# Performance work log

Measured on AMD Instinct MI355X. Metric: run time of the kernel, lower is better.

Reference implementation:

```python
import jax, jax.numpy as jnp
import numpy as np

ALPHA = 1000.0  # softmin temperature from the original module


def setup_inputs() -> dict:
    key = jax.random.key(0)
    ks = jax.random.split(key, 10)
    B, D, H, E, K = 8192, 784, 256, 32, 512
    s = 0.05  # small init scale to keep activations/distances numerically sane
    return {
        "x": jax.random.normal(ks[0], (B, D), jnp.float32),
        "cluster_reps": jax.random.normal(ks[1], (K, E), jnp.float32),
        "W1": jax.random.normal(ks[2], (D, H), jnp.float32) * s,
        "b1": jnp.zeros((H,), jnp.float32),
        "W2": jax.random.normal(ks[3], (H, E), jnp.float32) * s,
        "b2": jnp.zeros((E,), jnp.float32),
        "W3": jax.random.normal(ks[4], (E, H), jnp.float32) * s,
        "b3": jnp.zeros((H,), jnp.float32),
        "W4": jax.random.normal(ks[5], (H, D), jnp.float32) * s,
        "b4": jnp.zeros((D,), jnp.float32),
    }


def reference(x, cluster_reps, W1, b1, W2, b2, W3, b3, W4, b4):
    # --- autoencoder: 2-layer MLP encoder / decoder ---
    h = jax.nn.relu(x @ W1 + b1)            # [B, H]
    embeddings = h @ W2 + b2                # [B, E]
    h2 = jax.nn.relu(embeddings @ W3 + b3)  # [B, H]
    reconstruction = h2 @ W4 + b4           # [B, D]

    # --- squared distances to cluster reps: [B, K] ---
    diff = embeddings[:, None, :] - cluster_reps[None, :, :]  # [B, K, E]
    distances = jnp.sum(diff * diff, axis=2)                  # [B, K]

    # --- stable softmin-weighted distances ---
    min_dist = jnp.min(distances, axis=1, keepdims=True)       # [B, 1]
    exponentials = jnp.exp(-ALPHA * (distances - min_dist))    # [B, K]
    sum_exponentials = jnp.sum(exponentials, axis=1, keepdims=True)
    weighted_dists = distances * (exponentials / sum_exponentials)

    return (weighted_dists, distances, reconstruction, embeddings)
```

## Files before the change

### kernel.cpp

```cpp
#include <hip/hip_runtime.h>
#include <cstddef>

#define NB 8192
#define ND 784
#define NH 256
#define NE 32
#define NK 512
#define ALPHA_F 1000.0f

typedef _Float16 h8 __attribute__((ext_vector_type(8)));
typedef float f32x4 __attribute__((ext_vector_type(4)));

__global__ __launch_bounds__(256)
void splitw2_kernel(const float* __restrict__ W1, _Float16* __restrict__ w1thi,
                    _Float16* __restrict__ w1tlo,
                    const float* __restrict__ W4, _Float16* __restrict__ w4thi,
                    _Float16* __restrict__ w4tlo) {
    const int b = blockIdx.x;
    const float* W; _Float16 *hi, *lo; int K, N, n;
    if (b < NH) { W = W1; hi = w1thi; lo = w1tlo; K = ND; N = NH; n = b; }
    else        { W = W4; hi = w4thi; lo = w4tlo; K = NH; N = ND; n = b - NH; }
    for (int k = threadIdx.x; k < K; k += 256) {
        float w = W[(size_t)k * N + n];
        _Float16 hh = (_Float16)w;
        float r = w - (float)hh;
        hi[(size_t)n * K + k] = hh;
        lo[(size_t)n * K + k] = (_Float16)(r * 2048.0f);
    }
}

template<int TERMS, bool RELU, bool SPLITA, int MT>
__global__ __launch_bounds__(256)
void mfma_gemm3(const float* __restrict__ Af32,
                const _Float16* __restrict__ Ahi_g,
                const _Float16* __restrict__ Alo_g,
                const _Float16* __restrict__ WThi,
                const _Float16* __restrict__ WTlo,
                const float* __restrict__ bias, float* __restrict__ C,
                int N, int K, int KS) {
    constexpr int BM  = MT * 32;
    constexpr int ACH = BM / 64;

    __shared__ _Float16 sAhi[2][BM * 40];
    __shared__ _Float16 sAlo[2][BM * 40];
    __shared__ _Float16 sBhi[2][64 * 40];
    __shared__ _Float16 sBlo[2][64 * 40];

    const int tid = threadIdx.x;
    const int bm  = blockIdx.x * BM;
    const int bn  = blockIdx.y * 64;

    const int arow = (ACH == 1) ? (tid >> 2) : (tid >> 1);
    const int ak   = (ACH == 1) ? ((tid & 3) * 8) : ((tid & 1) * 16);
    const int brow = tid >> 2;
    const int bk   = (tid & 3) * 8;

    const float*    pA32 = SPLITA ? Af32 + (size_t)(bm + arow) * K : nullptr;
    const _Float16* pAhi = SPLITA ? nullptr : Ahi_g + (size_t)(bm + arow) * K;
    const _Float16* pAlo = SPLITA ? nullptr : Alo_g + (size_t)(bm + arow) * K;
    int brow_g = bn + brow; if (brow_g > N - 1) brow_g = N - 1;
    const _Float16* pBhi = WThi + (size_t)brow_g * K;
    const _Float16* pBlo = WTlo + (size_t)brow_g * K;

    float araw[ACH * 8];
    h8 rahi[ACH], ralo[ACH];
    h8 rbhi, rblo;

    auto prefetch = [&](int s) {
        #pragma unroll
        for (int c = 0; c < ACH; ++c) {
            const int k = s * 32 + ak + c * 8;
            if (SPLITA) {
                if (k + 8 <= K) {
                    f32x4 v0 = *(const f32x4*)(pA32 + k);
                    f32x4 v1 = *(const f32x4*)(pA32 + k + 4);
                    #pragma unroll
                    for (int j = 0; j < 4; ++j) {
                        araw[c * 8 + j]     = v0[j];
                        araw[c * 8 + 4 + j] = v1[j];
                    }
                } else {
                    #pragma unroll
                    for (int j = 0; j < 8; ++j) araw[c * 8 + j] = 0.f;
                }
            } else {
                rahi[c] = (k + 8 <= K) ? *(const h8*)(pAhi + k) : (h8){};
                ralo[c] = (k + 8 <= K) ? *(const h8*)(pAlo + k) : (h8){};
            }
        }
        const int kb = s * 32 + bk;
        rbhi = (kb + 8 <= K) ? *(const h8*)(pBhi + kb) : (h8){};
        rblo = (kb + 8 <= K) ? *(const h8*)(pBlo + kb) : (h8){};
    };

    auto commit = [&](int buf) {
        #pragma unroll
        for (int c = 0; c < ACH; ++c) {
            h8 hi, lo;
            if (SPLITA) {
                #pragma unroll
                for (int j = 0; j < 8; ++j) {
                    float v = araw[c * 8 + j];
                    _Float16 hh = (_Float16)v;
                    hi[j] = hh;
                    lo[j] = (_Float16)((v - (float)hh) * 2048.0f);
                }
            } else { hi = rahi[c]; lo = ralo[c]; }
            *(h8*)&sAhi[buf][arow * 40 + ak + c * 8] = hi;
            *(h8*)&sAlo[buf][arow * 40 + ak + c * 8] = lo;
        }
        *(h8*)&sBhi[buf][brow * 40 + bk] = rbhi;
        *(h8*)&sBlo[buf][brow * 40 + bk] = rblo;
    };

    prefetch(0);
    commit(0);
    prefetch(1);
    __syncthreads();

    const int lane = tid & 63;
    const int wv   = tid >> 6;
    const int wm   = (wv >> 1) * (MT * 16);
    const int wn   = (wv & 1) * 32;
    const int li   = lane & 15;
    const int kq   = (lane >> 4) * 8;

    f32x4 acc0[MT][2] = {};
    f32x4 acc1[MT][2] = {};
    f32x4 acc2[MT][2] = {};

    for (int s = 0; s < KS; ++s) {
        const int buf = s & 1;
        h8 fahi[MT], falo[MT], fbhi[2], fblo[2];
        #pragma unroll
        for (int mt = 0; mt < MT; ++mt) {
            const int ao = (wm + mt * 16 + li) * 40 + kq;
            fahi[mt] = *(const h8*)&sAhi[buf][ao];
            falo[mt] = *(const h8*)&sAlo[buf][ao];
        }
        #pragma unroll
        for (int nt = 0; nt < 2; ++nt) {
            const int bo = (wn + nt * 16 + li) * 40 + kq;
            fbhi[nt] = *(const h8*)&sBhi[buf][bo];
            fblo[nt] = *(const h8*)&sBlo[buf][bo];
        }
        #pragma unroll
        for (int mt = 0; mt < MT; ++mt)
            #pragma unroll
            for (int nt = 0; nt < 2; ++nt) {
                acc0[mt][nt] = __builtin_amdgcn_mfma_f32_16x16x32_f16(
                    fahi[mt], fbhi[nt], acc0[mt][nt], 0, 0, 0);
                acc1[mt][nt] = __builtin_amdgcn_mfma_f32_16x16x32_f16(
                    fahi[mt], fblo[nt], acc1[mt][nt], 0, 0, 0);
                acc1[mt][nt] = __builtin_amdgcn_mfma_f32_16x16x32_f16(
                    falo[mt], fbhi[nt], acc1[mt][nt], 0, 0, 0);
                if (TERMS == 4)
                    acc2[mt][nt] = __builtin_amdgcn_mfma_f32_16x16x32_f16(
                        falo[mt], fblo[nt], acc2[mt][nt], 0, 0, 0);
            }
        if (s + 1 < KS) {
            commit((s + 1) & 1);
            if (s + 2 < KS) prefetch(s + 2);
        }
        __syncthreads();
    }

    const float c1 = 1.0f / 2048.0f;
    const float c2 = c1 * c1;
    const int quad = lane >> 4;
    #pragma unroll
    for (int nt = 0; nt < 2; ++nt) {
        const int n = bn + wn + nt * 16 + li;
        if (n < N) {
            const float bv = bias[n];
            #pragma unroll
            for (int mt = 0; mt < MT; ++mt) {
                #pragma unroll
                for (int r = 0; r < 4; ++r) {
                    const int m = bm + wm + mt * 16 + quad * 4 + r;
                    float v = acc0[mt][nt][r] + c1 * acc1[mt][nt][r];
                    if (TERMS == 4) v += c2 * acc2[mt][nt][r];
                    v += bv;
                    if (RELU) v = fmaxf(v, 0.f);
                    C[(size_t)m * N + n] = v;
                }
            }
        }
    }
}

__global__ __launch_bounds__(256)
void mid_kernel(const float* __restrict__ h, const float* __restrict__ W2,
                const float* __restrict__ b2, const float* __restrict__ W3,
                const float* __restrict__ b3, float* __restrict__ emb,
                _Float16* __restrict__ h2hi, _Float16* __restrict__ h2lo) {
    __shared__ float es[16][32];
    const int tid = threadIdx.x;
    const int r0  = blockIdx.x * 16;

    #pragma unroll
    for (int half = 0; half < 2; ++half) {
        const int o   = tid + half * 256;
        const int row = o >> 5;
        const int col = o & 31;
        const float* hrow = h + (size_t)(r0 + row) * NH;
        float acc0 = 0.f, acc1 = 0.f;
        #pragma unroll 4
        for (int k = 0; k < NH; k += 4) {
            float4 hv = *(const float4*)(hrow + k);
            acc0 = fmaf(hv.x, W2[(k + 0) * NE + col], acc0);
            acc1 = fmaf(hv.y, W2[(k + 1) * NE + col], acc1);
            acc0 = fmaf(hv.z, W2[(k + 2) * NE + col], acc0);
            acc1 = fmaf(hv.w, W2[(k + 3) * NE + col], acc1);
        }
        float v = acc0 + acc1 + b2[col];
        es[row][col] = v;
        emb[(size_t)r0 * NE + o] = v;
    }
    __syncthreads();

    const int col = tid;
    float acc[16];
    #pragma unroll
    for (int r = 0; r < 16; ++r) acc[r] = 0.f;
    #pragma unroll
    for (int k = 0; k < NE; ++k) {
        float w = W3[k * NH + col];
        #pragma unroll
        for (int r = 0; r < 16; ++r) acc[r] = fmaf(es[r][k], w, acc[r]);
    }
    const float bb = b3[col];
    #pragma unroll
    for (int r = 0; r < 16; ++r) {
        float v = acc[r] + bb;
        v = v > 0.f ? v : 0.f;
        _Float16 hh = (_Float16)v;
        float rr = v - (float)hh;
        h2hi[(size_t)(r0 + r) * NH + col] = hh;
        h2lo[(size_t)(r0 + r) * NH + col] = (_Float16)(rr * 2048.0f);
    }
}

__global__ __launch_bounds__(512, 4)
void dist_kernel(const float* __restrict__ emb, const float* __restrict__ reps,
                 float* __restrict__ dist, float* __restrict__ wout) {
    __shared__ float es[8][32];
    __shared__ float tr[8][520];
    __shared__ float rmin[8];
    __shared__ float rinv[8];

    const int tid = threadIdx.x;
    const int r0  = blockIdx.x * 8;

    if (tid < 256) es[tid >> 5][tid & 31] = emb[(size_t)r0 * NE + tid];

    const float* rp = reps + (size_t)tid * NE;
    f32x4 rv[8];
    #pragma unroll
    for (int e4 = 0; e4 < 8; ++e4) rv[e4] = ((const f32x4*)rp)[e4];
    __syncthreads();

    float d[8];
    #pragma unroll
    for (int r = 0; r < 8; ++r) {
        float a = 0.f;
        #pragma unroll
        for (int e4 = 0; e4 < 8; ++e4) {
            f32x4 ev = *(const f32x4*)&es[r][e4 * 4];
            #pragma unroll
            for (int j = 0; j < 4; ++j) {
                float t = ev[j] - rv[e4][j];
                a = fmaf(t, t, a);
            }
        }
        d[r] = a;
    }

    const int lane = tid & 63;
    const int wv   = tid >> 6;

    #pragma unroll
    for (int r = 0; r < 8; ++r) tr[r][tid] = d[r];
    __syncthreads();
    {
        f32x4 a = *(const f32x4*)&tr[wv][lane * 8];
        f32x4 b = *(const f32x4*)&tr[wv][lane * 8 + 4];
        float m = fminf(fminf(fminf(a[0], a[1]), fminf(a[2], a[3])),
                        fminf(fminf(b[0], b[1]), fminf(b[2], b[3])));
        #pragma unroll
        for (int off = 32; off > 0; off >>= 1)
            m = fminf(m, __shfl_xor(m, off, 64));
        if (lane == 0) rmin[wv] = m;
    }
    __syncthreads();

    float e[8];
    #pragma unroll
    for (int r = 0; r < 8; ++r) {
        e[r] = expf(-ALPHA_F * (d[r] - rmin[r]));
        tr[r][tid] = e[r];
    }
    __syncthreads();
    {
        f32x4 a = *(const f32x4*)&tr[wv][lane * 8];
        f32x4 b = *(const f32x4*)&tr[wv][lane * 8 + 4];
        float s = ((a[0] + a[1]) + (a[2] + a[3])) +
                  ((b[0] + b[1]) + (b[2] + b[3]));
        #pragma unroll
        for (int off = 32; off > 0; off >>= 1)
            s += __shfl_xor(s, off, 64);
        if (lane == 0) rinv[wv] = 1.0f / s;
    }
    __syncthreads();

    #pragma unroll
    for (int r = 0; r < 8; ++r) {
        const size_t row = (size_t)(r0 + r);
        dist[row * NK + tid] = d[r];
        wout[row * NK + tid] = d[r] * (e[r] * rinv[r]);
    }
}

extern "C" void kernel_launch(void* const* d_in, const int* in_sizes, int n_in,
                              void* d_out, int out_size, void* d_ws, size_t ws_size,
                              hipStream_t stream) {
    const float* x    = (const float*)d_in[0];
    const float* reps = (const float*)d_in[1];
    const float* W1   = (const float*)d_in[2];
    const float* b1   = (const float*)d_in[3];
    const float* W2   = (const float*)d_in[4];
    const float* b2   = (const float*)d_in[5];
    const float* W3   = (const float*)d_in[6];
    const float* b3   = (const float*)d_in[7];
    const float* W4   = (const float*)d_in[8];
    const float* b4   = (const float*)d_in[9];

    float* out   = (float*)d_out;
    float* wout  = out;
    float* dist  = out + (size_t)NB * NK;
    float* recon = out + (size_t)2 * NB * NK;
    float* emb   = out + (size_t)2 * NB * NK + (size_t)NB * ND;

    float*    h     = dist;
    _Float16* h2hi  = (_Float16*)(dist + (size_t)NB * NH);
    _Float16* h2lo  = h2hi + (size_t)NB * NH;
    _Float16* w1thi = (_Float16*)wout;
    _Float16* w1tlo = w1thi + (size_t)NH * ND;
    _Float16* w4thi = w1tlo + (size_t)NH * ND;
    _Float16* w4tlo = w4thi + (size_t)ND * NH;

    splitw2_kernel<<<NH + ND, 256, 0, stream>>>(W1, w1thi, w1tlo,
                                                W4, w4thi, w4tlo);

    mfma_gemm3<4, true, true, 2><<<dim3(128, 4), 256, 0, stream>>>(
        x, nullptr, nullptr, w1thi, w1tlo, b1, h, NH, ND, 25);

    mid_kernel<<<NB / 16, 256, 0, stream>>>(h, W2, b2, W3, b3, emb, h2hi, h2lo);

    mfma_gemm3<3, false, false, 4><<<dim3(64, 13), 256, 0, stream>>>(
        nullptr, h2hi, h2lo, w4thi, w4tlo, b4, recon, ND, NH, 8);

    dist_kernel<<<NB / 8, 512, 0, stream>>>(emb, reps, dist, wout);
}
```

Before: 181.2 us.

## Fuse recon GEMM and distance/softmin into one heterogeneous tail kernel

Moves the split weights and h2 buffers into workspace so the distance kernel no longer has to wait for the recon GEMM to finish using the output buffers. Both can then run in one launch whose blocks interleave GEMM tiles and 256-thread distance tiles, overlapping the compute-bound GEMM with the memory-bound distance/softmin work. This saves one kernel launch and the tail of the GEMM. The cost is that every block reserves the larger GEMM shared-memory footprint and uses a uniform 256-thread size, which may lower occupancy for the distance blocks. It also depends on a large enough workspace, with the old path kept as a fallback.

```diff
diff --git a/kernel.cpp b/kernel.cpp
--- a/kernel.cpp
+++ b/kernel.cpp
@@ -30,25 +30,23 @@
 }
 
 template<int TERMS, bool RELU, bool SPLITA, int MT>
-__global__ __launch_bounds__(256)
-void mfma_gemm3(const float* __restrict__ Af32,
-                const _Float16* __restrict__ Ahi_g,
-                const _Float16* __restrict__ Alo_g,
-                const _Float16* __restrict__ WThi,
-                const _Float16* __restrict__ WTlo,
-                const float* __restrict__ bias, float* __restrict__ C,
-                int N, int K, int KS) {
+__device__ __forceinline__ void gemm_body(
+    const float* __restrict__ Af32,
+    const _Float16* __restrict__ Ahi_g,
+    const _Float16* __restrict__ Alo_g,
+    const _Float16* __restrict__ WThi,
+    const _Float16* __restrict__ WTlo,
+    const float* __restrict__ bias, float* __restrict__ C,
+    int N, int K, int KS, int bx, int by, int tid,
+    _Float16* __restrict__ sAhi, _Float16* __restrict__ sAlo,
+    _Float16* __restrict__ sBhi, _Float16* __restrict__ sBlo) {
     constexpr int BM  = MT * 32;
     constexpr int ACH = BM / 64;
-
-    __shared__ _Float16 sAhi[2][BM * 40];
-    __shared__ _Float16 sAlo[2][BM * 40];
-    __shared__ _Float16 sBhi[2][64 * 40];
-    __shared__ _Float16 sBlo[2][64 * 40];
-
-    const int tid = threadIdx.x;
-    const int bm  = blockIdx.x * BM;
-    const int bn  = blockIdx.y * 64;
+    constexpr int AS  = BM * 40;
+    constexpr int BS  = 64 * 40;
+
+    const int bm = bx * BM;
+    const int bn = by * 64;
 
     const int arow = (ACH == 1) ? (tid >> 2) : (tid >> 1);
     const int ak   = (ACH == 1) ? ((tid & 3) * 8) : ((tid & 1) * 16);
@@ -106,11 +104,11 @@
                     lo[j] = (_Float16)((v - (float)hh) * 2048.0f);
                 }
             } else { hi = rahi[c]; lo = ralo[c]; }
-            *(h8*)&sAhi[buf][arow * 40 + ak + c * 8] = hi;
-            *(h8*)&sAlo[buf][arow * 40 + ak + c * 8] = lo;
-        }
-        *(h8*)&sBhi[buf][brow * 40 + bk] = rbhi;
-        *(h8*)&sBlo[buf][brow * 40 + bk] = rblo;
+            *(h8*)&sAhi[buf * AS + arow * 40 + ak + c * 8] = hi;
+            *(h8*)&sAlo[buf * AS + arow * 40 + ak + c * 8] = lo;
+        }
+        *(h8*)&sBhi[buf * BS + brow * 40 + bk] = rbhi;
+        *(h8*)&sBlo[buf * BS + brow * 40 + bk] = rblo;
     };
 
     prefetch(0);
@@ -134,15 +132,15 @@
         h8 fahi[MT], falo[MT], fbhi[2], fblo[2];
         #pragma unroll
         for (int mt = 0; mt < MT; ++mt) {
-            const int ao = (wm + mt * 16 + li) * 40 + kq;
-            fahi[mt] = *(const h8*)&sAhi[buf][ao];
-            falo[mt] = *(const h8*)&sAlo[buf][ao];
+            const int ao = buf * AS + (wm + mt * 16 + li) * 40 + kq;
+            fahi[mt] = *(const h8*)&sAhi[ao];
+            falo[mt] = *(const h8*)&sAlo[ao];
         }
         #pragma unroll
         for (int nt = 0; nt < 2; ++nt) {
-            const int bo = (wn + nt * 16 + li) * 40 + kq;
-            fbhi[nt] = *(const h8*)&sBhi[buf][bo];
-            fblo[nt] = *(const h8*)&sBlo[buf][bo];
+            const int bo = buf * BS + (wn + nt * 16 + li) * 40 + kq;
+            fbhi[nt] = *(const h8*)&sBhi[bo];
+            fblo[nt] = *(const h8*)&sBlo[bo];
         }
         #pragma unroll
         for (int mt = 0; mt < MT; ++mt)
@@ -189,6 +187,26 @@
     }
 }
 
+template<int TERMS, bool RELU, bool SPLITA, int MT>
+__global__ __launch_bounds__(256)
+void mfma_gemm3(const float* __restrict__ Af32,
+                const _Float16* __restrict__ Ahi_g,
+                const _Float16* __restrict__ Alo_g,
+                const _Float16* __restrict__ WThi,
+                const _Float16* __restrict__ WTlo,
+                const float* __restrict__ bias, float* __restrict__ C,
+                int N, int K, int KS) {
+    constexpr int BM = MT * 32;
+    __shared__ __align__(16) _Float16 smem[2 * BM * 40 * 2 + 2 * 64 * 40 * 2];
+    _Float16* sAhi = smem;
+    _Float16* sAlo = sAhi + 2 * BM * 40;
+    _Float16* sBhi = sAlo + 2 * BM * 40;
+    _Float16* sBlo = sBhi + 2 * 64 * 40;
+    gemm_body<TERMS, RELU, SPLITA, MT>(Af32, Ahi_g, Alo_g, WThi, WTlo, bias, C,
+                                       N, K, KS, blockIdx.x, blockIdx.y,
+                                       threadIdx.x, sAhi, sAlo, sBhi, sBlo);
+}
+
 __global__ __launch_bounds__(256)
 void mid_kernel(const float* __restrict__ h, const float* __restrict__ W2,
                 const float* __restrict__ b2, const float* __restrict__ W3,
@@ -241,6 +259,98 @@
     }
 }
 
+__device__ __forceinline__ void dist_body256(
+    const float* __restrict__ emb, const float* __restrict__ reps,
+    float* __restrict__ dist, float* __restrict__ wout,
+    int blk, int tid, float* __restrict__ es, float* __restrict__ tr,
+    float* __restrict__ rmin, float* __restrict__ rinv) {
+    const int r0 = blk * 8;
+    es[tid] = emb[(size_t)r0 * NE + tid];
+
+    const float* rp0 = reps + (size_t)tid * NE;
+    const float* rp1 = reps + (size_t)(tid + 256) * NE;
+    f32x4 rv0[8], rv1[8];
+    #pragma unroll
+    for (int e4 = 0; e4 < 8; ++e4) {
+        rv0[e4] = ((const f32x4*)rp0)[e4];
+        rv1[e4] = ((const f32x4*)rp1)[e4];
+    }
+    __syncthreads();
+
+    float d0[8], d1[8];
+    #pragma unroll
+    for (int r = 0; r < 8; ++r) {
+        float a0 = 0.f, a1 = 0.f;
+        #pragma unroll
+        for (int e4 = 0; e4 < 8; ++e4) {
+            f32x4 ev = *(const f32x4*)&es[r * 32 + e4 * 4];
+            #pragma unroll
+            for (int j = 0; j < 4; ++j) {
+                float t0 = ev[j] - rv0[e4][j];
+                a0 = fmaf(t0, t0, a0);
+                float t1 = ev[j] - rv1[e4][j];
+                a1 = fmaf(t1, t1, a1);
+            }
+        }
+        d0[r] = a0; d1[r] = a1;
+    }
+
+    const int lane = tid & 63;
+    const int wv   = tid >> 6;
+
+    #pragma unroll
+    for (int r = 0; r < 8; ++r) {
+        tr[r * 520 + tid]       = d0[r];
+        tr[r * 520 + 256 + tid] = d1[r];
+    }
+    __syncthreads();
+    #pragma unroll
+    for (int p = 0; p < 2; ++p) {
+        const int rr = wv + p * 4;
+        f32x4 a = *(const f32x4*)&tr[rr * 520 + lane * 8];
+        f32x4 b = *(const f32x4*)&tr[rr * 520 + lane * 8 + 4];
+        float m = fminf(fminf(fminf(a[0], a[1]), fminf(a[2], a[3])),
+                        fminf(fminf(b[0], b[1]), fminf(b[2], b[3])));
+        #pragma unroll
+        for (int off = 32; off > 0; off >>= 1)
+            m = fminf(m, __shfl_xor(m, off, 64));
+        if (lane == 0) rmin[rr] = m;
+    }
+    __syncthreads();
+
+    float e0[8], e1[8];
+    #pragma unroll
+    for (int r = 0; r < 8; ++r) {
+        e0[r] = expf(-ALPHA_F * (d0[r] - rmin[r]));
+        e1[r] = expf(-ALPHA_F * (d1[r] - rmin[r]));
+        tr[r * 520 + tid]       = e0[r];
+        tr[r * 520 + 256 + tid] = e1[r];
+    }
+    __syncthreads();
+    #pragma unroll
+    for (int p = 0; p < 2; ++p) {
+        const int rr = wv + p * 4;
+        f32x4 a = *(const f32x4*)&tr[rr * 520 + lane * 8];
+        f32x4 b = *(const f32x4*)&tr[rr * 520 + lane * 8 + 4];
+        float s = ((a[0] + a[1]) + (a[2] + a[3])) +
+                  ((b[0] + b[1]) + (b[2] + b[3]));
+        #pragma unroll
+        for (int off = 32; off > 0; off >>= 1)
+            s += __shfl_xor(s, off, 64);
+        if (lane == 0) rinv[rr] = 1.0f / s;
+    }
+    __syncthreads();
+
+    #pragma unroll
+    for (int r = 0; r < 8; ++r) {
+        const size_t row = (size_t)(r0 + r);
+        dist[row * NK + tid]       = d0[r];
+        dist[row * NK + 256 + tid] = d1[r];
+        wout[row * NK + tid]       = d0[r] * (e0[r] * rinv[r]);
+        wout[row * NK + 256 + tid] = d1[r] * (e1[r] * rinv[r]);
+    }
+}
+
 __global__ __launch_bounds__(512, 4)
 void dist_kernel(const float* __restrict__ emb, const float* __restrict__ reps,
                  float* __restrict__ dist, float* __restrict__ wout) {
@@ -318,6 +428,42 @@
         const size_t row = (size_t)(r0 + r);
         dist[row * NK + tid] = d[r];
         wout[row * NK + tid] = d[r] * (e[r] * rinv[r]);
+    }
+}
+
+#define NGB (64 * 13)
+#define NDB (NB / 8)
+
+__global__ __launch_bounds__(256)
+void tail_fused(const _Float16* __restrict__ h2hi,
+                const _Float16* __restrict__ h2lo,
+                const _Float16* __restrict__ w4thi,
+                const _Float16* __restrict__ w4tlo,
+                const float* __restrict__ b4, float* __restrict__ recon,
+                const float* __restrict__ emb, const float* __restrict__ reps,
+                float* __restrict__ dist, float* __restrict__ wout) {
+    __shared__ __align__(16) _Float16 smem[2 * 128 * 40 * 2 + 2 * 64 * 40 * 2];
+    const int bid = blockIdx.x;
+    const int tid = threadIdx.x;
+
+    bool isDist; int idx;
+    if (bid < 2 * NGB) { isDist = (bid & 1); idx = bid >> 1; }
+    else               { isDist = true; idx = NGB + (bid - 2 * NGB); }
+
+    if (!isDist) {
+        _Float16* sAhi = smem;
+        _Float16* sAlo = sAhi + 2 * 128 * 40;
+        _Float16* sBhi = sAlo + 2 * 128 * 40;
+        _Float16* sBlo = sBhi + 2 * 64 * 40;
+        gemm_body<3, false, false, 4>(nullptr, h2hi, h2lo, w4thi, w4tlo, b4,
+                                      recon, ND, NH, 8, idx & 63, idx >> 6,
+                                      tid, sAhi, sAlo, sBhi, sBlo);
+    } else {
+        float* es   = (float*)smem;
+        float* tr   = es + 8 * 32;
+        float* rmin = tr + 8 * 520;
+        float* rinv = rmin + 8;
+        dist_body256(emb, reps, dist, wout, idx, tid, es, tr, rmin, rinv);
     }
 }
 
@@ -341,24 +487,43 @@
     float* recon = out + (size_t)2 * NB * NK;
     float* emb   = out + (size_t)2 * NB * NK + (size_t)NB * ND;
 
-    float*    h     = dist;
-    _Float16* h2hi  = (_Float16*)(dist + (size_t)NB * NH);
-    _Float16* h2lo  = h2hi + (size_t)NB * NH;
-    _Float16* w1thi = (_Float16*)wout;
-    _Float16* w1tlo = w1thi + (size_t)NH * ND;
-    _Float16* w4thi = w1tlo + (size_t)NH * ND;
-    _Float16* w4tlo = w4thi + (size_t)ND * NH;
-
-    splitw2_kernel<<<NH + ND, 256, 0, stream>>>(W1, w1thi, w1tlo,
-                                                W4, w4thi, w4tlo);
-
-    mfma_gemm3<4, true, true, 2><<<dim3(128, 4), 256, 0, stream>>>(
-        x, nullptr, nullptr, w1thi, w1tlo, b1, h, NH, ND, 25);
-
-    mid_kernel<<<NB / 16, 256, 0, stream>>>(h, W2, b2, W3, b3, emb, h2hi, h2lo);
-
-    mfma_gemm3<3, false, false, 4><<<dim3(64, 13), 256, 0, stream>>>(
-        nullptr, h2hi, h2lo, w4thi, w4tlo, b4, recon, ND, NH, 8);
-
-    dist_kernel<<<NB / 8, 512, 0, stream>>>(emb, reps, dist, wout);
-}
+    float* h = dist;
+
+    const size_t wneed = ((size_t)4 * ND * NH + (size_t)2 * NB * NH)
+                         * sizeof(_Float16);
+
+    if (d_ws != nullptr && ws_size >= wneed) {
+        _Float16* w1thi = (_Float16*)d_ws;
+        _Float16* w1tlo = w1thi + (size_t)NH * ND;
+        _Float16* w4thi = w1tlo + (size_t)NH * ND;
+        _Float16* w4tlo = w4thi + (size_t)ND * NH;
+        _Float16* h2hi  = w4tlo + (size_t)ND * NH;
+        _Float16* h2lo  = h2hi + (size_t)NB * NH;
+
+        splitw2_kernel<<<NH + ND, 256, 0, stream>>>(W1, w1thi, w1tlo,
+                                                    W4, w4thi, w4tlo);
+        mfma_gemm3<4, true, true, 2><<<dim3(128, 4), 256, 0, stream>>>(
+            x, nullptr, nullptr, w1thi, w1tlo, b1, h, NH, ND, 25);
+        mid_kernel<<<NB / 16, 256, 0, stream>>>(h, W2, b2, W3, b3,
+                                                emb, h2hi, h2lo);
+        tail_fused<<<2 * NGB + (NDB - NGB), 256, 0, stream>>>(
+            h2hi, h2lo, w4thi, w4tlo, b4, recon, emb, reps, dist, wout);
+    } else {
+        _Float16* h2hi  = (_Float16*)(dist + (size_t)NB * NH);
+        _Float16* h2lo  = h2hi + (size_t)NB * NH;
+        _Float16* w1thi = (_Float16*)wout;
+        _Float16* w1tlo = w1thi + (size_t)NH * ND;
+        _Float16* w4thi = w1tlo + (size_t)NH * ND;
+        _Float16* w4tlo = w4thi + (size_t)ND * NH;
+
+        splitw2_kernel<<<NH + ND, 256, 0, stream>>>(W1, w1thi, w1tlo,
+                                                    W4, w4thi, w4tlo);
+        mfma_gemm3<4, true, true, 2><<<dim3(128, 4), 256, 0, stream>>>(
+            x, nullptr, nullptr, w1thi, w1tlo, b1, h, NH, ND, 25);
+        mid_kernel<<<NB / 16, 256, 0, stream>>>(h, W2, b2, W3, b3,
+                                                emb, h2hi, h2lo);
+        mfma_gemm3<3, false, false, 4><<<dim3(64, 13), 256, 0, stream>>>(
+            nullptr, h2hi, h2lo, w4thi, w4tlo, b4, recon, ND, NH, 8);
+        dist_kernel<<<NB / 8, 512, 0, stream>>>(emb, reps, dist, wout);
+    }
+}
```

Result: faster. 176.9 us (-2.4%).

## Fuse entire autoencoder and softmin pipeline into one persistent mega kernel

Applied to the files above, without the earlier changes.

Replaces the chain of four kernels with one prep kernel that splits all four weight matrices into fp16 hi/lo pairs in workspace using an LDS-tiled transpose, plus a single fused kernel. Each 512-thread block owns 32 rows and runs the encoder, embedding, decoder GEMMs and the distance/softmin stage entirely in LDS. This removes intermediate global round-trips (h, h2, emb reload) and launch gaps, at the cost of very large LDS use, one block per CU, only 256 blocks, and recomputing W4 tile loads per block. The old path remains as a fallback when no workspace is available.

```diff
diff --git a/kernel.cpp b/kernel.cpp
--- a/kernel.cpp
+++ b/kernel.cpp
@@ -10,6 +10,434 @@
 
 typedef _Float16 h8 __attribute__((ext_vector_type(8)));
 typedef float f32x4 __attribute__((ext_vector_type(4)));
+
+#define TW1 25
+#define TN1 8
+#define NBW1 200
+#define TW4 8
+#define TN4 25
+#define NBW4 200
+#define NBW2 8
+#define NBW3 8
+
+__global__ __launch_bounds__(256)
+void prep4_kernel(const float* __restrict__ W1, _Float16* __restrict__ w1thi,
+                  _Float16* __restrict__ w1tlo,
+                  const float* __restrict__ W4, _Float16* __restrict__ w4thi,
+                  _Float16* __restrict__ w4tlo,
+                  const float* __restrict__ W2, _Float16* __restrict__ w2thi,
+                  _Float16* __restrict__ w2tlo,
+                  const float* __restrict__ W3, _Float16* __restrict__ w3thi,
+                  _Float16* __restrict__ w3tlo) {
+    __shared__ float tile[32][33];
+    const int b   = blockIdx.x;
+    const int tid = threadIdx.x;
+
+    const float* W; _Float16 *hi, *lo; int K, N, kt, nt;
+    if (b < NBW1) {
+        W = W1; hi = w1thi; lo = w1tlo; K = ND; N = NH;
+        kt = b % TW1; nt = b / TW1;
+    } else if (b < NBW1 + NBW4) {
+        const int bb = b - NBW1;
+        W = W4; hi = w4thi; lo = w4tlo; K = NH; N = ND;
+        kt = bb % TW4; nt = bb / TW4;
+    } else if (b < NBW1 + NBW4 + NBW2) {
+        W = W2; hi = w2thi; lo = w2tlo; K = NH; N = NE;
+        kt = b - (NBW1 + NBW4); nt = 0;
+    } else {
+        W = W3; hi = w3thi; lo = w3tlo; K = NE; N = NH;
+        kt = 0; nt = b - (NBW1 + NBW4 + NBW2);
+    }
+    const int k0 = kt * 32, n0 = nt * 32;
+    const int row = tid >> 3, c4 = (tid & 7) * 4;
+    #pragma unroll
+    for (int j = 0; j < 4; ++j) {
+        const int k = k0 + row, n = n0 + c4 + j;
+        tile[row][c4 + j] = (k < K && n < N) ? W[(size_t)k * N + n] : 0.f;
+    }
+    __syncthreads();
+    const int n = n0 + row;
+    if (n < N) {
+        #pragma unroll
+        for (int j = 0; j < 4; ++j) {
+            const int k = k0 + c4 + j;
+            if (k < K) {
+                float w = tile[c4 + j][row];
+                _Float16 hh = (_Float16)w;
+                float r = w - (float)hh;
+                hi[(size_t)n * K + k] = hh;
+                lo[(size_t)n * K + k] = (_Float16)(r * 2048.0f);
+            }
+        }
+    }
+}
+
+__global__ __launch_bounds__(512, 1)
+void mega_kernel(const float* __restrict__ x, const float* __restrict__ reps,
+                 const _Float16* __restrict__ w1thi, const _Float16* __restrict__ w1tlo,
+                 const _Float16* __restrict__ w2thi, const _Float16* __restrict__ w2tlo,
+                 const _Float16* __restrict__ w3thi, const _Float16* __restrict__ w3tlo,
+                 const _Float16* __restrict__ w4thi, const _Float16* __restrict__ w4tlo,
+                 const float* __restrict__ b1, const float* __restrict__ b2,
+                 const float* __restrict__ b3, const float* __restrict__ b4,
+                 float* __restrict__ emb_g, float* __restrict__ recon_g,
+                 float* __restrict__ dist_g, float* __restrict__ wout_g) {
+    __shared__ __align__(16) unsigned char lds[135936];
+    _Float16* R0h  = (_Float16*)lds;
+    _Float16* sA   = (_Float16*)(lds + 81920);
+    _Float16* hP   = (_Float16*)(lds + 92160);
+    float*    es   = (float*)(lds + 125952);
+    _Float16* eP   = (_Float16*)(lds + 130560);
+    float*    rmin = (float*)(lds + 135680);
+    float*    rinv = (float*)(lds + 135808);
+
+    const int tid  = threadIdx.x;
+    const int lane = tid & 63;
+    const int wv   = tid >> 6;
+    const int li   = lane & 15;
+    const int kq   = (lane >> 4) * 8;
+    const int quad = lane >> 4;
+    const int r0   = blockIdx.x * 32;
+
+    const float c1 = 1.0f / 2048.0f;
+    const float c2 = c1 * c1;
+
+    {
+        _Float16* sBhi = R0h;
+        _Float16* sBlo = R0h + 2 * 256 * 40;
+        _Float16* sAhi = sA;
+        _Float16* sAlo = sA + 2 * 32 * 40;
+        const int arow = (tid & 127) >> 2;
+        const int ak   = (tid & 3) * 8;
+        const int brow = tid >> 1;
+        const int bk   = (tid & 1) * 16;
+        const float*    pA  = x + (size_t)(r0 + arow) * ND;
+        const _Float16* pBh = w1thi + (size_t)brow * ND;
+        const _Float16* pBl = w1tlo + (size_t)brow * ND;
+
+        float araw[8];
+        h8 rb0, rb1, rb2, rb3;
+
+        auto pf = [&](int s) {
+            if (tid < 128) {
+                const int k = s * 32 + ak;
+                if (k + 8 <= ND) {
+                    f32x4 v0 = *(const f32x4*)(pA + k);
+                    f32x4 v1 = *(const f32x4*)(pA + k + 4);
+                    #pragma unroll
+                    for (int j = 0; j < 4; ++j) {
+                        araw[j] = v0[j]; araw[4 + j] = v1[j];
+                    }
+                } else {
+                    #pragma unroll
+                    for (int j = 0; j < 8; ++j) araw[j] = 0.f;
+                }
+            }
+            const int kb = s * 32 + bk;
+            rb0 = (kb + 8  <= ND) ? *(const h8*)(pBh + kb)     : (h8){};
+            rb1 = (kb + 16 <= ND) ? *(const h8*)(pBh + kb + 8) : (h8){};
+            rb2 = (kb + 8  <= ND) ? *(const h8*)(pBl + kb)     : (h8){};
+            rb3 = (kb + 16 <= ND) ? *(const h8*)(pBl + kb + 8) : (h8){};
+        };
+        auto cm = [&](int buf) {
+            if (tid < 128) {
+                h8 hi, lo;
+                #pragma unroll
+                for (int j = 0; j < 8; ++j) {
+                    float v = araw[j];
+                    _Float16 hh = (_Float16)v;
+                    hi[j] = hh;
+                    lo[j] = (_Float16)((v - (float)hh) * 2048.0f);
+                }
+                *(h8*)&sAhi[buf * 32 * 40 + arow * 40 + ak] = hi;
+                *(h8*)&sAlo[buf * 32 * 40 + arow * 40 + ak] = lo;
+            }
+            *(h8*)&sBhi[buf * 256 * 40 + brow * 40 + bk]     = rb0;
+            *(h8*)&sBhi[buf * 256 * 40 + brow * 40 + bk + 8] = rb1;
+            *(h8*)&sBlo[buf * 256 * 40 + brow * 40 + bk]     = rb2;
+            *(h8*)&sBlo[buf * 256 * 40 + brow * 40 + bk + 8] = rb3;
+        };
+
+        pf(0); cm(0); pf(1);
+        __syncthreads();
+
+        f32x4 a0[2][2] = {}, a1[2][2] = {}, a2[2][2] = {};
+        for (int s = 0; s < 25; ++s) {
+            const int buf = s & 1;
+            h8 fah[2], fal[2], fbh[2], fbl[2];
+            #pragma unroll
+            for (int mt = 0; mt < 2; ++mt) {
+                const int ao = buf * 32 * 40 + (mt * 16 + li) * 40 + kq;
+                fah[mt] = *(const h8*)&sAhi[ao];
+                fal[mt] = *(const h8*)&sAlo[ao];
+            }
+            #pragma unroll
+            for (int nt = 0; nt < 2; ++nt) {
+                const int bo = buf * 256 * 40 + (wv * 32 + nt * 16 + li) * 40 + kq;
+                fbh[nt] = *(const h8*)&sBhi[bo];
+                fbl[nt] = *(const h8*)&sBlo[bo];
+            }
+            #pragma unroll
+            for (int mt = 0; mt < 2; ++mt)
+                #pragma unroll
+                for (int nt = 0; nt < 2; ++nt) {
+                    a0[mt][nt] = __builtin_amdgcn_mfma_f32_16x16x32_f16(
+                        fah[mt], fbh[nt], a0[mt][nt], 0, 0, 0);
+                    a1[mt][nt] = __builtin_amdgcn_mfma_f32_16x16x32_f16(
+                        fah[mt], fbl[nt], a1[mt][nt], 0, 0, 0);
+                    a1[mt][nt] = __builtin_amdgcn_mfma_f32_16x16x32_f16(
+                        fal[mt], fbh[nt], a1[mt][nt], 0, 0, 0);
+                    a2[mt][nt] = __builtin_amdgcn_mfma_f32_16x16x32_f16(
+                        fal[mt], fbl[nt], a2[mt][nt], 0, 0, 0);
+                }
+            if (s + 1 < 25) { cm((s + 1) & 1); if (s + 2 < 25) pf(s + 2); }
+            __syncthreads();
+        }
+        _Float16* hhi = hP;
+        _Float16* hlo = hP + 32 * 264;
+        #pragma unroll
+        for (int nt = 0; nt < 2; ++nt) {
+            const int n = wv * 32 + nt * 16 + li;
+            const float bv = b1[n];
+            #pragma unroll
+            for (int mt = 0; mt < 2; ++mt)
+                #pragma unroll
+                for (int r = 0; r < 4; ++r) {
+                    const int m = mt * 16 + quad * 4 + r;
+                    float v = a0[mt][nt][r] + c1 * a1[mt][nt][r]
+                            + c2 * a2[mt][nt][r] + bv;
+                    v = fmaxf(v, 0.f);
+                    _Float16 hh = (_Float16)v;
+                    hhi[m * 264 + n] = hh;
+                    hlo[m * 264 + n] = (_Float16)((v - (float)hh) * 2048.0f);
+                }
+        }
+    }
+    __syncthreads();
+
+    {
+        _Float16* w2h = R0h;
+        _Float16* w2l = R0h + 32 * 264;
+        #pragma unroll
+        for (int i = 0; i < 2; ++i) {
+            const int cc  = tid + i * 512;
+            const int row = cc >> 5, off = (cc & 31) * 8;
+            *(h8*)&w2h[row * 264 + off] = *(const h8*)(w2thi + row * 256 + off);
+            *(h8*)&w2l[row * 264 + off] = *(const h8*)(w2tlo + row * 256 + off);
+        }
+    }
+    __syncthreads();
+    if (wv < 4) {
+        const int mt = wv >> 1, nt = wv & 1;
+        _Float16* hhi = hP;
+        _Float16* hlo = hP + 32 * 264;
+        _Float16* w2h = R0h;
+        _Float16* w2l = R0h + 32 * 264;
+        f32x4 e0 = {}, e1 = {}, e2 = {};
+        #pragma unroll
+        for (int ks = 0; ks < 8; ++ks) {
+            h8 ah = *(const h8*)&hhi[(mt * 16 + li) * 264 + ks * 32 + kq];
+            h8 al = *(const h8*)&hlo[(mt * 16 + li) * 264 + ks * 32 + kq];
+            h8 bh = *(const h8*)&w2h[(nt * 16 + li) * 264 + ks * 32 + kq];
+            h8 bl = *(const h8*)&w2l[(nt * 16 + li) * 264 + ks * 32 + kq];
+            e0 = __builtin_amdgcn_mfma_f32_16x16x32_f16(ah, bh, e0, 0, 0, 0);
+            e1 = __builtin_amdgcn_mfma_f32_16x16x32_f16(ah, bl, e1, 0, 0, 0);
+            e1 = __builtin_amdgcn_mfma_f32_16x16x32_f16(al, bh, e1, 0, 0, 0);
+            e2 = __builtin_amdgcn_mfma_f32_16x16x32_f16(al, bl, e2, 0, 0, 0);
+        }
+        const int ccol = nt * 16 + li;
+        const float bv = b2[ccol];
+        _Float16* ehi = eP;
+        _Float16* elo = eP + 32 * 40;
+        #pragma unroll
+        for (int r = 0; r < 4; ++r) {
+            const int m = mt * 16 + quad * 4 + r;
+            float v = e0[r] + c1 * e1[r] + c2 * e2[r] + bv;
+            es[m * 36 + ccol] = v;
+            _Float16 hh = (_Float16)v;
+            ehi[m * 40 + ccol] = hh;
+            elo[m * 40 + ccol] = (_Float16)((v - (float)hh) * 2048.0f);
+            emb_g[(size_t)(r0 + m) * NE + ccol] = v;
+        }
+    }
+    __syncthreads();
+
+    {
+        _Float16* w3h = R0h;
+        _Float16* w3l = R0h + 256 * 40;
+        #pragma unroll
+        for (int i = 0; i < 2; ++i) {
+            const int cc  = tid + i * 512;
+            const int row = cc >> 2, off = (cc & 3) * 8;
+            *(h8*)&w3h[row * 40 + off] = *(const h8*)(w3thi + row * 32 + off);
+            *(h8*)&w3l[row * 40 + off] = *(const h8*)(w3tlo + row * 32 + off);
+        }
+    }
+    __syncthreads();
+    {
+        const int n0 = wv * 32;
+        _Float16* w3h  = R0h;
+        _Float16* w3l  = R0h + 256 * 40;
+        _Float16* ehi  = eP;
+        _Float16* elo  = eP + 32 * 40;
+        _Float16* h2hi = hP;
+        _Float16* h2lo = hP + 32 * 264;
+        h8 ah[2], al[2];
+        #pragma unroll
+        for (int mt = 0; mt < 2; ++mt) {
+            ah[mt] = *(const h8*)&ehi[(mt * 16 + li) * 40 + kq];
+            al[mt] = *(const h8*)&elo[(mt * 16 + li) * 40 + kq];
+        }
+        #pragma unroll
+        for (int nt = 0; nt < 2; ++nt) {
+            h8 bh = *(const h8*)&w3h[(n0 + nt * 16 + li) * 40 + kq];
+            h8 bl = *(const h8*)&w3l[(n0 + nt * 16 + li) * 40 + kq];
+            const int col = n0 + nt * 16 + li;
+            const float bv = b3[col];
+            #pragma unroll
+            for (int mt = 0; mt < 2; ++mt) {
+                f32x4 q0 = {}, q1 = {}, q2 = {};
+                q0 = __builtin_amdgcn_mfma_f32_16x16x32_f16(ah[mt], bh, q0, 0, 0, 0);
+                q1 = __builtin_amdgcn_mfma_f32_16x16x32_f16(ah[mt], bl, q1, 0, 0, 0);
+                q1 = __builtin_amdgcn_mfma_f32_16x16x32_f16(al[mt], bh, q1, 0, 0, 0);
+                q2 = __builtin_amdgcn_mfma_f32_16x16x32_f16(al[mt], bl, q2, 0, 0, 0);
+                #pragma unroll
+                for (int r = 0; r < 4; ++r) {
+                    const int m = mt * 16 + quad * 4 + r;
+                    float v = q0[r] + c1 * q1[r] + c2 * q2[r] + bv;
+                    v = fmaxf(v, 0.f);
+                    _Float16 hh = (_Float16)v;
+                    h2hi[m * 264 + col] = hh;
+                    h2lo[m * 264 + col] = (_Float16)((v - (float)hh) * 2048.0f);
+                }
+            }
+        }
+    }
+    __syncthreads();
+
+    {
+        _Float16* sBhi = R0h;
+        _Float16* sBlo = R0h + 2 * 128 * 40;
+        _Float16* h2hi = hP;
+        _Float16* h2lo = hP + 32 * 264;
+        const int brow = tid >> 2;
+        const int bk4  = (tid & 3) * 8;
+        h8 rbh, rbl;
+        auto pf = [&](int ss) {
+            int rg = (ss >> 3) * 128 + brow;
+            if (rg > ND - 1) rg = ND - 1;
+            const int k = (ss & 7) * 32 + bk4;
+            rbh = *(const h8*)(w4thi + (size_t)rg * NH + k);
+            rbl = *(const h8*)(w4tlo + (size_t)rg * NH + k);
+        };
+        auto cm = [&](int ss) {
+            const int buf = ss & 1;
+            *(h8*)&sBhi[buf * 128 * 40 + brow * 40 + bk4] = rbh;
+            *(h8*)&sBlo[buf * 128 * 40 + brow * 40 + bk4] = rbl;
+        };
+        pf(0); cm(0); pf(1);
+        __syncthreads();
+
+        f32x4 q0[2] = {}, q1[2] = {};
+        for (int ss = 0; ss < 56; ++ss) {
+            const int buf = ss & 1, ks = ss & 7;
+            h8 fbh = *(const h8*)&sBhi[buf * 128 * 40 + (wv * 16 + li) * 40 + kq];
+            h8 fbl = *(const h8*)&sBlo[buf * 128 * 40 + (wv * 16 + li) * 40 + kq];
+            #pragma unroll
+            for (int mt = 0; mt < 2; ++mt) {
+                h8 ah = *(const h8*)&h2hi[(mt * 16 + li) * 264 + ks * 32 + kq];
+                h8 al = *(const h8*)&h2lo[(mt * 16 + li) * 264 + ks * 32 + kq];
+                q0[mt] = __builtin_amdgcn_mfma_f32_16x16x32_f16(ah, fbh, q0[mt], 0, 0, 0);
+                q1[mt] = __builtin_amdgcn_mfma_f32_16x16x32_f16(ah, fbl, q1[mt], 0, 0, 0);
+                q1[mt] = __builtin_amdgcn_mfma_f32_16x16x32_f16(al, fbh, q1[mt], 0, 0, 0);
+            }
+            if (ss + 1 < 56) { cm(ss + 1); if (ss + 2 < 56) pf(ss + 2); }
+            __syncthreads();
+            if (ks == 7) {
+                const int n = (ss >> 3) * 128 + wv * 16 + li;
+                if (n < ND) {
+                    const float bv = b4[n];
+                    #pragma unroll
+                    for (int mt = 0; mt < 2; ++mt)
+                        #pragma unroll
+                        for (int r = 0; r < 4; ++r) {
+                            const int m = mt * 16 + quad * 4 + r;
+                            recon_g[(size_t)(r0 + m) * ND + n] =
+                                q0[mt][r] + c1 * q1[mt][r] + bv;
+                        }
+                }
+                #pragma unroll
+                for (int mt = 0; mt < 2; ++mt) { q0[mt] = {}; q1[mt] = {}; }
+            }
+        }
+    }
+    __syncthreads();
+
+    {
+        float* tr = (float*)R0h;
+        const float* rp = reps + (size_t)tid * NE;
+        f32x4 rv[8];
+        #pragma unroll
+        for (int e4 = 0; e4 < 8; ++e4) rv[e4] = ((const f32x4*)rp)[e4];
+
+        float d[32];
+        #pragma unroll
+        for (int r = 0; r < 32; ++r) {
+            float a = 0.f;
+            #pragma unroll
+            for (int e4 = 0; e4 < 8; ++e4) {
+                f32x4 ev = *(const f32x4*)&es[r * 36 + e4 * 4];
+                #pragma unroll
+                for (int j = 0; j < 4; ++j) {
+                    float t = ev[j] - rv[e4][j];
+                    a = fmaf(t, t, a);
+                }
+            }
+            d[r] = a;
+            tr[r * 520 + tid] = a;
+        }
+        __syncthreads();
+        #pragma unroll
+        for (int p = 0; p < 4; ++p) {
+            const int rr = wv * 4 + p;
+            f32x4 a = *(const f32x4*)&tr[rr * 520 + lane * 8];
+            f32x4 b = *(const f32x4*)&tr[rr * 520 + lane * 8 + 4];
+            float m = fminf(fminf(fminf(a[0], a[1]), fminf(a[2], a[3])),
+                            fminf(fminf(b[0], b[1]), fminf(b[2], b[3])));
+            #pragma unroll
+            for (int off = 32; off > 0; off >>= 1)
+                m = fminf(m, __shfl_xor(m, off, 64));
+            if (lane == 0) rmin[rr] = m;
+        }
+        __syncthreads();
+        float e[32];
+        #pragma unroll
+        for (int r = 0; r < 32; ++r) {
+            e[r] = expf(-ALPHA_F * (d[r] - rmin[r]));
+            tr[r * 520 + tid] = e[r];
+        }
+        __syncthreads();
+        #pragma unroll
+        for (int p = 0; p < 4; ++p) {
+            const int rr = wv * 4 + p;
+            f32x4 a = *(const f32x4*)&tr[rr * 520 + lane * 8];
+            f32x4 b = *(const f32x4*)&tr[rr * 520 + lane * 8 + 4];
+            float s = ((a[0] + a[1]) + (a[2] + a[3])) +
+                      ((b[0] + b[1]) + (b[2] + b[3]));
+            #pragma unroll
+            for (int off = 32; off > 0; off >>= 1)
+                s += __shfl_xor(s, off, 64);
+            if (lane == 0) rinv[rr] = 1.0f / s;
+        }
+        __syncthreads();
+        #pragma unroll
+        for (int r = 0; r < 32; ++r) {
+            const size_t row = (size_t)(r0 + r);
+            dist_g[row * NK + tid] = d[r];
+            wout_g[row * NK + tid] = d[r] * (e[r] * rinv[r]);
+        }
+    }
+}
 
 __global__ __launch_bounds__(256)
 void splitw2_kernel(const float* __restrict__ W1, _Float16* __restrict__ w1thi,
@@ -40,11 +468,13 @@
                 int N, int K, int KS) {
     constexpr int BM  = MT * 32;
     constexpr int ACH = BM / 64;
-
-    __shared__ _Float16 sAhi[2][BM * 40];
-    __shared__ _Float16 sAlo[2][BM * 40];
-    __shared__ _Float16 sBhi[2][64 * 40];
-    __shared__ _Float16 sBlo[2][64 * 40];
+    constexpr int AS  = BM * 40;
+    constexpr int BS  = 64 * 40;
+    __shared__ __align__(16) _Float16 smem[2 * BM * 40 * 2 + 2 * 64 * 40 * 2];
+    _Float16* sAhi = smem;
+    _Float16* sAlo = sAhi + 2 * BM * 40;
+    _Float16* sBhi = sAlo + 2 * BM * 40;
+    _Float16* sBlo = sBhi + 2 * 64 * 40;
 
     const int tid = threadIdx.x;
     const int bm  = blockIdx.x * BM;
@@ -106,11 +536,11 @@
                     lo[j] = (_Float16)((v - (float)hh) * 2048.0f);
                 }
             } else { hi = rahi[c]; lo = ralo[c]; }
-            *(h8*)&sAhi[buf][arow * 40 + ak + c * 8] = hi;
-            *(h8*)&sAlo[buf][arow * 40 + ak + c * 8] = lo;
-        }
-        *(h8*)&sBhi[buf][brow * 40 + bk] = rbhi;
-        *(h8*)&sBlo[buf][brow * 40 + bk] = rblo;
+            *(h8*)&sAhi[buf * AS + arow * 40 + ak + c * 8] = hi;
+            *(h8*)&sAlo[buf * AS + arow * 40 + ak + c * 8] = lo;
+        }
+        *(h8*)&sBhi[buf * BS + brow * 40 + bk] = rbhi;
+        *(h8*)&sBlo[buf * BS + brow * 40 + bk] = rblo;
     };
 
     prefetch(0);
@@ -134,15 +564,15 @@
         h8 fahi[MT], falo[MT], fbhi[2], fblo[2];
         #pragma unroll
         for (int mt = 0; mt < MT; ++mt) {
-            const int ao = (wm + mt * 16 + li) * 40 + kq;
-            fahi[mt] = *(const h8*)&sAhi[buf][ao];
-            falo[mt] = *(const h8*)&sAlo[buf][ao];
+            const int ao = buf * AS + (wm + mt * 16 + li) * 40 + kq;
+            fahi[mt] = *(const h8*)&sAhi[ao];
+            falo[mt] = *(const h8*)&sAlo[ao];
         }
         #pragma unroll
         for (int nt = 0; nt < 2; ++nt) {
-            const int bo = (wn + nt * 16 + li) * 40 + kq;
-            fbhi[nt] = *(const h8*)&sBhi[buf][bo];
-            fblo[nt] = *(const h8*)&sBlo[buf][bo];
+            const int bo = buf * BS + (wn + nt * 16 + li) * 40 + kq;
+            fbhi[nt] = *(const h8*)&sBhi[bo];
+            fblo[nt] = *(const h8*)&sBlo[bo];
         }
         #pragma unroll
         for (int mt = 0; mt < MT; ++mt)
@@ -341,24 +771,44 @@
     float* recon = out + (size_t)2 * NB * NK;
     float* emb   = out + (size_t)2 * NB * NK + (size_t)NB * ND;
 
-    float*    h     = dist;
-    _Float16* h2hi  = (_Float16*)(dist + (size_t)NB * NH);
-    _Float16* h2lo  = h2hi + (size_t)NB * NH;
-    _Float16* w1thi = (_Float16*)wout;
-    _Float16* w1tlo = w1thi + (size_t)NH * ND;
-    _Float16* w4thi = w1tlo + (size_t)NH * ND;
-    _Float16* w4tlo = w4thi + (size_t)ND * NH;
-
-    splitw2_kernel<<<NH + ND, 256, 0, stream>>>(W1, w1thi, w1tlo,
-                                                W4, w4thi, w4tlo);
-
-    mfma_gemm3<4, true, true, 2><<<dim3(128, 4), 256, 0, stream>>>(
-        x, nullptr, nullptr, w1thi, w1tlo, b1, h, NH, ND, 25);
-
-    mid_kernel<<<NB / 16, 256, 0, stream>>>(h, W2, b2, W3, b3, emb, h2hi, h2lo);
-
-    mfma_gemm3<3, false, false, 4><<<dim3(64, 13), 256, 0, stream>>>(
-        nullptr, h2hi, h2lo, w4thi, w4tlo, b4, recon, ND, NH, 8);
-
-    dist_kernel<<<NB / 8, 512, 0, stream>>>(emb, reps, dist, wout);
+    const size_t nW14 = (size_t)ND * NH;
+    const size_t nW23 = (size_t)NE * NH;
+    const size_t wneed = (4 * nW14 + 4 * nW23) * sizeof(_Float16);
+
+    if (d_ws != nullptr && ws_size >= wneed) {
+        _Float16* w1thi = (_Float16*)d_ws;
+        _Float16* w1tlo = w1thi + nW14;
+        _Float16* w4thi = w1tlo + nW14;
+        _Float16* w4tlo = w4thi + nW14;
+        _Float16* w2thi = w4tlo + nW14;
+        _Float16* w2tlo = w2thi + nW23;
+        _Float16* w3thi = w2tlo + nW23;
+        _Float16* w3tlo = w3thi + nW23;
+
+        prep4_kernel<<<NBW1 + NBW4 + NBW2 + NBW3, 256, 0, stream>>>(
+            W1, w1thi, w1tlo, W4, w4thi, w4tlo,
+            W2, w2thi, w2tlo, W3, w3thi, w3tlo);
+
+        mega_kernel<<<NB / 32, 512, 0, stream>>>(
+            x, reps, w1thi, w1tlo, w2thi, w2tlo, w3thi, w3tlo, w4thi, w4tlo,
+            b1, b2, b3, b4, emb, recon, dist, wout);
+    } else {
+        float* h = dist;
+        _Float16* h2hi  = (_Float16*)(dist + (size_t)NB * NH);
+        _Float16* h2lo  = h2hi + (size_t)NB * NH;
+        _Float16* w1thi = (_Float16*)wout;
+        _Float16* w1tlo = w1thi + (size_t)NH * ND;
+        _Float16* w4thi = w1tlo + (size_t)NH * ND;
+        _Float16* w4tlo = w4thi + (size_t)ND * NH;
+
+        splitw2_kernel<<<NH + ND, 256, 0, stream>>>(W1, w1thi, w1tlo,
+                                                    W4, w4thi, w4tlo);
+        mfma_gemm3<4, true, true, 2><<<dim3(128, 4), 256, 0, stream>>>(
+            x, nullptr, nullptr, w1thi, w1tlo, b1, h, NH, ND, 25);
+        mid_kernel<<<NB / 16, 256, 0, stream>>>(h, W2, b2, W3, b3,
+                                                emb, h2hi, h2lo);
+        mfma_gemm3<3, false, false, 4><<<dim3(64, 13), 256, 0, stream>>>(
+            nullptr, h2hi, h2lo, w4thi, w4tlo, b4, recon, ND, NH, 8);
+        dist_kernel<<<NB / 8, 512, 0, stream>>>(emb, reps, dist, wout);
+    }
 }
```

After: 166.1 us. 1.09x faster.
